# Optimization experiments

Measured on AMD Instinct MI355X. Metric: run time of the kernel, lower is better.

## Reference

```python
import jax, jax.numpy as jnp
import numpy as np

L = 2048      # seq_len
E = 2048      # hidden_dim
H = 16        # num_heads
D = E // H    # head_dim


def setup_inputs() -> dict:
    key = jax.random.key(0)
    ks = jax.random.split(key, 6)
    x = jax.random.normal(ks[0], (L, E), dtype=jnp.float32)
    bias_matrix = jax.random.normal(ks[1], (L, L), dtype=jnp.float32) * 0.1
    # nn.MultiheadAttention params: packed in_proj [3E, E] + bias [3E], out_proj [E, E] + bias [E]
    in_proj_weight = jax.random.normal(ks[2], (3 * E, E), dtype=jnp.float32) * 0.02
    in_proj_bias = jax.random.normal(ks[3], (3 * E,), dtype=jnp.float32) * 0.02
    out_proj_weight = jax.random.normal(ks[4], (E, E), dtype=jnp.float32) * 0.02
    out_proj_bias = jax.random.normal(ks[5], (E,), dtype=jnp.float32) * 0.02
    return {
        "x": x,
        "bias_matrix": bias_matrix,
        "in_proj_weight": in_proj_weight,
        "in_proj_bias": in_proj_bias,
        "out_proj_weight": out_proj_weight,
        "out_proj_bias": out_proj_bias,
    }


def reference(x, bias_matrix, in_proj_weight, in_proj_bias, out_proj_weight, out_proj_bias):
    # Packed QKV projection (torch Linear convention: y = x @ W.T + b)
    qkv = x @ in_proj_weight.T + in_proj_bias            # [L, 3E]
    q, k, v = jnp.split(qkv, 3, axis=-1)                 # each [L, E]
    q = q.reshape(L, H, D)
    k = k.reshape(L, H, D)
    v = v.reshape(L, H, D)
    scale = 1.0 / jnp.sqrt(jnp.asarray(D, dtype=x.dtype))
    # scores: [H, L, L]; bias_matrix broadcast over heads (torch 2D attn_mask semantics)
    scores = jnp.einsum("lhd,mhd->hlm", q * scale, k) + bias_matrix[None, :, :]
    attn = jax.nn.softmax(scores, axis=-1)
    ctx = jnp.einsum("hlm,mhd->lhd", attn, v).reshape(L, E)
    out = ctx @ out_proj_weight.T + out_proj_bias        # [L, E]
    return out
```

## Files before the change

### kernel.cpp

```cpp
#include <hip/hip_runtime.h>
#include <math.h>

#define L_SEQ 2048
#define E_DIM 2048
#define H_NUM 16
#define D_HEAD 128

typedef __attribute__((ext_vector_type(8))) _Float16 half8;
typedef __attribute__((ext_vector_type(4))) _Float16 half4;
typedef __attribute__((ext_vector_type(4))) float floatx4;

static __device__ __forceinline__ void gload16(const void* g, void* lds) {
  __builtin_amdgcn_global_load_lds(
      (const __attribute__((address_space(1))) void*)g,
      (__attribute__((address_space(3))) void*)lds, 16, 0, 0);
}

__global__ __launch_bounds__(256)
void cvt3_f32_f16(const float* __restrict__ a, _Float16* __restrict__ oa, int na,
                  const float* __restrict__ b, _Float16* __restrict__ ob, int nb,
                  const float* __restrict__ c, _Float16* __restrict__ oc, int nc) {
  int i = (blockIdx.x * 256 + threadIdx.x) * 8;
  const float* src;
  _Float16* dst;
  if (i < na) {
    src = a + i; dst = oa + i;
  } else if (i < na + nb) {
    src = b + (i - na); dst = ob + (i - na);
  } else if (i < na + nb + nc) {
    src = c + (i - na - nb); dst = oc + (i - na - nb);
  } else {
    return;
  }
  float4 p = *(const float4*)src;
  float4 q = *(const float4*)(src + 4);
  half8 h = {(_Float16)p.x, (_Float16)p.y, (_Float16)p.z, (_Float16)p.w,
             (_Float16)q.x, (_Float16)q.y, (_Float16)q.z, (_Float16)q.w};
  *(half8*)dst = h;
}

template <int TM, int TN, int WR, int WC, int EPI>
__global__ __launch_bounds__(256)
void gemm_mfma(const _Float16* __restrict__ A, const _Float16* __restrict__ B,
               const float* __restrict__ bias, float* __restrict__ C,
               _Float16* __restrict__ qk, _Float16* __restrict__ vt,
               int M, int N, int K) {
  constexpr int RT = TM / (16 * WR);
  constexpr int CT = TN / (16 * WC);
  constexpr int ACH = TM / 8;
  constexpr int NCH = (TM + TN) / 32;

  __shared__ _Float16 As[TM * 64];
  __shared__ _Float16 Bs[TN * 64];

  const int tid = threadIdx.x;
  const int wave = tid >> 6, lane = tid & 63;
  const int l15 = lane & 15, quad = lane >> 4;
  const int wr = wave / WC, wc = wave % WC;
  const int row0 = blockIdx.y * TM, col0 = blockIdx.x * TN;

  const int srow = lane >> 3;
  const int gc = (lane & 7) ^ srow;

  floatx4 acc[RT][CT];
#pragma unroll
  for (int i = 0; i < RT; ++i)
#pragma unroll
    for (int j = 0; j < CT; ++j) acc[i][j] = (floatx4){0.f, 0.f, 0.f, 0.f};

  for (int k0 = 0; k0 < K; k0 += 64) {
    __syncthreads();
#pragma unroll
    for (int c = 0; c < NCH; ++c) {
      int chunk = wave * NCH + c;
      if (chunk < ACH) {
        int row = chunk * 8 + srow;
        gload16((const char*)(A + (size_t)(row0 + row) * K + k0) + gc * 16,
                (char*)As + chunk * 1024);
      } else {
        int bch = chunk - ACH;
        int row = bch * 8 + srow;
        gload16((const char*)(B + (size_t)(col0 + row) * K + k0) + gc * 16,
                (char*)Bs + bch * 1024);
      }
    }
    __syncthreads();

#pragma unroll
    for (int ks = 0; ks < 2; ++ks) {
      half8 af[RT], bf[CT];
#pragma unroll
      for (int t = 0; t < RT; ++t) {
        int r = wr * (16 * RT) + t * 16 + l15;
        af[t] = *(const half8*)&As[r * 64 + (((ks * 4 + quad) ^ (r & 7)) * 8)];
      }
#pragma unroll
      for (int t = 0; t < CT; ++t) {
        int r = wc * (16 * CT) + t * 16 + l15;
        bf[t] = *(const half8*)&Bs[r * 64 + (((ks * 4 + quad) ^ (r & 7)) * 8)];
      }
#pragma unroll
      for (int tr = 0; tr < RT; ++tr)
#pragma unroll
        for (int tc = 0; tc < CT; ++tc)
          acc[tr][tc] = __builtin_amdgcn_mfma_f32_16x16x32_f16(
              af[tr], bf[tc], acc[tr][tc], 0, 0, 0);
    }
  }

  const int crow = row0 + wr * (16 * RT);
  const int ccol = col0 + wc * (16 * CT);

  if (EPI == 0) {
#pragma unroll
    for (int tc = 0; tc < CT; ++tc) {
      int col = ccol + tc * 16 + l15;
      float bb = bias[col];
#pragma unroll
      for (int tr = 0; tr < RT; ++tr)
#pragma unroll
        for (int r = 0; r < 4; ++r)
          C[(size_t)(crow + tr * 16 + quad * 4 + r) * N + col] =
              acc[tr][tc][r] + bb;
    }
  } else if (col0 < 2 * E_DIM) {
#pragma unroll
    for (int tc = 0; tc < CT; ++tc) {
      int col = ccol + tc * 16 + l15;
      float bb = bias[col];
#pragma unroll
      for (int tr = 0; tr < RT; ++tr)
#pragma unroll
        for (int r = 0; r < 4; ++r)
          qk[(size_t)(crow + tr * 16 + quad * 4 + r) * (2 * E_DIM) + col] =
              (_Float16)(acc[tr][tc][r] + bb);
    }
  } else {
#pragma unroll
    for (int tc = 0; tc < CT; ++tc) {
      int col = ccol + tc * 16 + l15;
      float bb = bias[col];
      int vrow = col - 2 * E_DIM;
#pragma unroll
      for (int tr = 0; tr < RT; ++tr) {
        int rbase = crow + tr * 16 + quad * 4;
        half4 h = {(_Float16)(acc[tr][tc][0] + bb), (_Float16)(acc[tr][tc][1] + bb),
                   (_Float16)(acc[tr][tc][2] + bb), (_Float16)(acc[tr][tc][3] + bb)};
        *(half4*)&vt[(size_t)vrow * L_SEQ + rbase] = h;
      }
    }
  }
}

__global__ __launch_bounds__(256, 1)
void attn_mfma(const _Float16* __restrict__ qk, const _Float16* __restrict__ vt,
               const float* __restrict__ bias, _Float16* __restrict__ ctx) {
  const int h = blockIdx.y;
  const int q0 = blockIdx.x * 128;
  const int tid = threadIdx.x;
  const int wave = tid >> 6;
  const int lane = tid & 63;
  const int l15 = lane & 15;
  const int quad = lane >> 4;

  __shared__ _Float16 Ks[64][136];
  __shared__ _Float16 Vst[128][72];
  __shared__ _Float16 Ps[128][72];

  half8 qa[2][4];
#pragma unroll
  for (int rt = 0; rt < 2; ++rt) {
    const _Float16* qp = qk + (size_t)(q0 + wave * 32 + rt * 16 + l15) * (2 * E_DIM) +
                         h * D_HEAD + quad * 8;
#pragma unroll
    for (int ks = 0; ks < 4; ++ks) qa[rt][ks] = *(const half8*)(qp + ks * 32);
  }

  float l_i[2][4];
#pragma unroll
  for (int rt = 0; rt < 2; ++rt)
#pragma unroll
    for (int r = 0; r < 4; ++r) l_i[rt][r] = 0.f;
  floatx4 o[2][8];
#pragma unroll
  for (int rt = 0; rt < 2; ++rt)
#pragma unroll
    for (int t = 0; t < 8; ++t) o[rt][t] = (floatx4){0.f, 0.f, 0.f, 0.f};

  const float scale = 0.088388347648318447f;

  half8 kreg[4], vreg[4];
  float breg[2][4][4], breg2[2][4][4];
#pragma unroll
  for (int c = 0; c < 4; ++c) {
    int m = c * 256 + tid;
    kreg[c] = *(const half8*)(qk + (size_t)(0 + (m >> 4)) * (2 * E_DIM) + E_DIM +
                              h * D_HEAD + (m & 15) * 8);
    vreg[c] = *(const half8*)(vt + (size_t)(h * D_HEAD + (m >> 3)) * L_SEQ + 0 +
                              (m & 7) * 8);
  }
#pragma unroll
  for (int rt = 0; rt < 2; ++rt)
#pragma unroll
    for (int t = 0; t < 4; ++t)
#pragma unroll
      for (int r = 0; r < 4; ++r)
        breg[rt][t][r] = bias[(size_t)(q0 + wave * 32 + rt * 16 + quad * 4 + r) *
                                  L_SEQ + 16 * t + l15];

#pragma unroll 2
  for (int kt = 0; kt < L_SEQ; kt += 64) {
    __syncthreads();
#pragma unroll
    for (int c = 0; c < 4; ++c) {
      int m = c * 256 + tid;
      *(half8*)&Ks[m >> 4][(m & 15) * 8] = kreg[c];
      *(half8*)&Vst[m >> 3][(m & 7) * 8] = vreg[c];
    }
    __syncthreads();

    if (kt + 64 < L_SEQ) {
#pragma unroll
      for (int c = 0; c < 4; ++c) {
        int m = c * 256 + tid;
        kreg[c] = *(const half8*)(qk + (size_t)(kt + 64 + (m >> 4)) * (2 * E_DIM) +
                                  E_DIM + h * D_HEAD + (m & 15) * 8);
        vreg[c] = *(const half8*)(vt + (size_t)(h * D_HEAD + (m >> 3)) * L_SEQ +
                                  kt + 64 + (m & 7) * 8);
      }
#pragma unroll
      for (int rt = 0; rt < 2; ++rt)
#pragma unroll
        for (int t = 0; t < 4; ++t)
#pragma unroll
          for (int r = 0; r < 4; ++r)
            breg2[rt][t][r] =
                bias[(size_t)(q0 + wave * 32 + rt * 16 + quad * 4 + r) * L_SEQ +
                     kt + 64 + 16 * t + l15];
    }

    floatx4 s[2][4];
#pragma unroll
    for (int t = 0; t < 4; ++t) {
      floatx4 a0 = (floatx4){0.f, 0.f, 0.f, 0.f};
      floatx4 a1 = (floatx4){0.f, 0.f, 0.f, 0.f};
#pragma unroll
      for (int ks = 0; ks < 4; ++ks) {
        half8 b = *(const half8*)&Ks[16 * t + l15][ks * 32 + quad * 8];
        a0 = __builtin_amdgcn_mfma_f32_16x16x32_f16(qa[0][ks], b, a0, 0, 0, 0);
        a1 = __builtin_amdgcn_mfma_f32_16x16x32_f16(qa[1][ks], b, a1, 0, 0, 0);
      }
      s[0][t] = a0;
      s[1][t] = a1;
    }

#pragma unroll
    for (int rt = 0; rt < 2; ++rt)
#pragma unroll
      for (int t = 0; t < 4; ++t)
#pragma unroll
        for (int r = 0; r < 4; ++r) {
          float p = __expf(fmaf(s[rt][t][r], scale, breg[rt][t][r]));
          s[rt][t][r] = p;
          Ps[wave * 32 + rt * 16 + quad * 4 + r][16 * t + l15] = (_Float16)p;
        }
#pragma unroll
    for (int rt = 0; rt < 2; ++rt)
#pragma unroll
      for (int r = 0; r < 4; ++r) {
        float ls = s[rt][0][r] + s[rt][1][r] + s[rt][2][r] + s[rt][3][r];
        ls += __shfl_xor(ls, 1);
        ls += __shfl_xor(ls, 2);
        ls += __shfl_xor(ls, 4);
        ls += __shfl_xor(ls, 8);
        l_i[rt][r] += ls;
      }

    half8 pa[2][2];
#pragma unroll
    for (int rt = 0; rt < 2; ++rt)
#pragma unroll
      for (int ks = 0; ks < 2; ++ks)
        pa[rt][ks] = *(const half8*)&Ps[wave * 32 + rt * 16 + l15][ks * 32 + quad * 8];
#pragma unroll
    for (int t = 0; t < 8; ++t) {
#pragma unroll
      for (int ks = 0; ks < 2; ++ks) {
        half8 b = *(const half8*)&Vst[16 * t + l15][ks * 32 + quad * 8];
        o[0][t] = __builtin_amdgcn_mfma_f32_16x16x32_f16(pa[0][ks], b, o[0][t], 0, 0, 0);
        o[1][t] = __builtin_amdgcn_mfma_f32_16x16x32_f16(pa[1][ks], b, o[1][t], 0, 0, 0);
      }
    }

#pragma unroll
    for (int rt = 0; rt < 2; ++rt)
#pragma unroll
      for (int t = 0; t < 4; ++t)
#pragma unroll
        for (int r = 0; r < 4; ++r) breg[rt][t][r] = breg2[rt][t][r];
  }

#pragma unroll
  for (int rt = 0; rt < 2; ++rt) {
    float inv_l[4];
#pragma unroll
    for (int r = 0; r < 4; ++r) inv_l[r] = 1.f / l_i[rt][r];
#pragma unroll
    for (int t = 0; t < 8; ++t)
#pragma unroll
      for (int r = 0; r < 4; ++r) {
        int row = q0 + wave * 32 + rt * 16 + quad * 4 + r;
        ctx[(size_t)row * E_DIM + h * D_HEAD + 16 * t + l15] =
            (_Float16)(o[rt][t][r] * inv_l[r]);
      }
  }
}

extern "C" void kernel_launch(void* const* d_in, const int* in_sizes, int n_in,
                              void* d_out, int out_size, void* d_ws, size_t ws_size,
                              hipStream_t stream) {
  const float* x          = (const float*)d_in[0];
  const float* bias_mat   = (const float*)d_in[1];
  const float* in_proj_w  = (const float*)d_in[2];
  const float* in_proj_b  = (const float*)d_in[3];
  const float* out_proj_w = (const float*)d_in[4];
  const float* out_proj_b = (const float*)d_in[5];
  float* out = (float*)d_out;

  _Float16* x16 = (_Float16*)d_ws;
  _Float16* w1  = x16 + (size_t)L_SEQ * E_DIM;
  _Float16* w2  = w1 + (size_t)3 * E_DIM * E_DIM;
  _Float16* qk  = w2 + (size_t)E_DIM * E_DIM;
  _Float16* vt  = qk + (size_t)L_SEQ * 2 * E_DIM;
  _Float16* ctx = vt + (size_t)E_DIM * L_SEQ;

  dim3 blk(256);
  const int nx = L_SEQ * E_DIM, nw1 = 3 * E_DIM * E_DIM, nw2 = E_DIM * E_DIM;

  cvt3_f32_f16<<<(nx + nw1 + nw2) / 2048, blk, 0, stream>>>(
      x, x16, nx, in_proj_w, w1, nw1, out_proj_w, w2, nw2);

  gemm_mfma<128, 128, 2, 2, 1><<<dim3(3 * E_DIM / 128, L_SEQ / 128), blk, 0, stream>>>(
      x16, w1, in_proj_b, nullptr, qk, vt, L_SEQ, 3 * E_DIM, E_DIM);

  attn_mfma<<<dim3(L_SEQ / 128, H_NUM), blk, 0, stream>>>(qk, vt, bias_mat, ctx);

  gemm_mfma<128, 64, 4, 1, 0><<<dim3(E_DIM / 64, L_SEQ / 128), blk, 0, stream>>>(
      ctx, w2, out_proj_b, out, nullptr, nullptr, L_SEQ, E_DIM, E_DIM);
}
```

Measured before the change: 342.5 us.

## Split attention over two key halves and merge partial results in a combine kernel

```diff
diff --git a/kernel.cpp b/kernel.cpp
--- a/kernel.cpp
+++ b/kernel.cpp
@@ -152,11 +152,15 @@
   }
 }
 
-__global__ __launch_bounds__(256, 1)
+__global__ __launch_bounds__(256, 2)
 void attn_mfma(const _Float16* __restrict__ qk, const _Float16* __restrict__ vt,
-               const float* __restrict__ bias, _Float16* __restrict__ ctx) {
+               const float* __restrict__ bias, _Float16* __restrict__ o_part,
+               float* __restrict__ l_part) {
   const int h = blockIdx.y;
   const int q0 = blockIdx.x * 128;
+  const int z = blockIdx.z;
+  const int kbase = z * (L_SEQ / 2);
+  const int kend = kbase + (L_SEQ / 2);
   const int tid = threadIdx.x;
   const int wave = tid >> 6;
   const int lane = tid & 63;
@@ -194,9 +198,9 @@
 #pragma unroll
   for (int c = 0; c < 4; ++c) {
     int m = c * 256 + tid;
-    kreg[c] = *(const half8*)(qk + (size_t)(0 + (m >> 4)) * (2 * E_DIM) + E_DIM +
+    kreg[c] = *(const half8*)(qk + (size_t)(kbase + (m >> 4)) * (2 * E_DIM) + E_DIM +
                               h * D_HEAD + (m & 15) * 8);
-    vreg[c] = *(const half8*)(vt + (size_t)(h * D_HEAD + (m >> 3)) * L_SEQ + 0 +
+    vreg[c] = *(const half8*)(vt + (size_t)(h * D_HEAD + (m >> 3)) * L_SEQ + kbase +
                               (m & 7) * 8);
   }
 #pragma unroll
@@ -206,10 +210,10 @@
 #pragma unroll
       for (int r = 0; r < 4; ++r)
         breg[rt][t][r] = bias[(size_t)(q0 + wave * 32 + rt * 16 + quad * 4 + r) *
-                                  L_SEQ + 16 * t + l15];
+                                  L_SEQ + kbase + 16 * t + l15];
 
 #pragma unroll 2
-  for (int kt = 0; kt < L_SEQ; kt += 64) {
+  for (int kt = kbase; kt < kend; kt += 64) {
     __syncthreads();
 #pragma unroll
     for (int c = 0; c < 4; ++c) {
@@ -219,7 +223,7 @@
     }
     __syncthreads();
 
-    if (kt + 64 < L_SEQ) {
+    if (kt + 64 < kend) {
 #pragma unroll
       for (int c = 0; c < 4; ++c) {
         int m = c * 256 + tid;
@@ -302,18 +306,40 @@
 
 #pragma unroll
   for (int rt = 0; rt < 2; ++rt) {
-    float inv_l[4];
-#pragma unroll
-    for (int r = 0; r < 4; ++r) inv_l[r] = 1.f / l_i[rt][r];
 #pragma unroll
     for (int t = 0; t < 8; ++t)
 #pragma unroll
       for (int r = 0; r < 4; ++r) {
         int row = q0 + wave * 32 + rt * 16 + quad * 4 + r;
-        ctx[(size_t)row * E_DIM + h * D_HEAD + 16 * t + l15] =
-            (_Float16)(o[rt][t][r] * inv_l[r]);
-      }
-  }
+        o_part[((size_t)z * L_SEQ + row) * E_DIM + h * D_HEAD + 16 * t + l15] =
+            (_Float16)o[rt][t][r];
+      }
+    if (l15 == 0) {
+#pragma unroll
+      for (int r = 0; r < 4; ++r) {
+        int row = q0 + wave * 32 + rt * 16 + quad * 4 + r;
+        l_part[((size_t)z * H_NUM + h) * L_SEQ + row] = l_i[rt][r];
+      }
+    }
+  }
+}
+
+__global__ __launch_bounds__(256)
+void attn_combine(const _Float16* __restrict__ o_part,
+                  const float* __restrict__ l_part, _Float16* __restrict__ ctx) {
+  size_t i = ((size_t)blockIdx.x * 256 + threadIdx.x) * 8;
+  int q = (int)(i / E_DIM);
+  int col = (int)(i % E_DIM);
+  int h = col >> 7;
+  float l = l_part[h * L_SEQ + q] + l_part[(size_t)H_NUM * L_SEQ + h * L_SEQ + q];
+  float inv = 1.f / l;
+  half8 a = *(const half8*)(o_part + i);
+  half8 b = *(const half8*)(o_part + (size_t)L_SEQ * E_DIM + i);
+  half8 o;
+#pragma unroll
+  for (int k = 0; k < 8; ++k)
+    o[k] = (_Float16)(((float)a[k] + (float)b[k]) * inv);
+  *(half8*)(ctx + i) = o;
 }
 
 extern "C" void kernel_launch(void* const* d_in, const int* in_sizes, int n_in,
@@ -333,6 +359,8 @@
   _Float16* qk  = w2 + (size_t)E_DIM * E_DIM;
   _Float16* vt  = qk + (size_t)L_SEQ * 2 * E_DIM;
   _Float16* ctx = vt + (size_t)E_DIM * L_SEQ;
+  float* l_part = (float*)(ctx + (size_t)L_SEQ * E_DIM);
+  _Float16* o_part = x16;
 
   dim3 blk(256);
   const int nx = L_SEQ * E_DIM, nw1 = 3 * E_DIM * E_DIM, nw2 = E_DIM * E_DIM;
@@ -343,7 +371,10 @@
   gemm_mfma<128, 128, 2, 2, 1><<<dim3(3 * E_DIM / 128, L_SEQ / 128), blk, 0, stream>>>(
       x16, w1, in_proj_b, nullptr, qk, vt, L_SEQ, 3 * E_DIM, E_DIM);
 
-  attn_mfma<<<dim3(L_SEQ / 128, H_NUM), blk, 0, stream>>>(qk, vt, bias_mat, ctx);
+  attn_mfma<<<dim3(L_SEQ / 128, H_NUM, 2), blk, 0, stream>>>(qk, vt, bias_mat,
+                                                             o_part, l_part);
+
+  attn_combine<<<(L_SEQ * E_DIM) / 2048, blk, 0, stream>>>(o_part, l_part, ctx);
 
   gemm_mfma<128, 64, 4, 1, 0><<<dim3(E_DIM / 64, L_SEQ / 128), blk, 0, stream>>>(
       ctx, w2, out_proj_b, out, nullptr, nullptr, L_SEQ, E_DIM, E_DIM);
```

Result: slower. 397.2 us (+16.0%).

## Double-buffer K/V tiles, transpose score MFMA, and read bias as fp16

Applied to the files above, without the earlier changes.

```diff
diff --git a/kernel.cpp b/kernel.cpp
--- a/kernel.cpp
+++ b/kernel.cpp
@@ -39,6 +39,17 @@
   *(half8*)dst = h;
 }
 
+__global__ __launch_bounds__(256)
+void cvt_f32_f16(const float* __restrict__ in, _Float16* __restrict__ out, int n) {
+  int i = (blockIdx.x * 256 + threadIdx.x) * 8;
+  if (i >= n) return;
+  float4 a = *(const float4*)(in + i);
+  float4 b = *(const float4*)(in + i + 4);
+  half8 h = {(_Float16)a.x, (_Float16)a.y, (_Float16)a.z, (_Float16)a.w,
+             (_Float16)b.x, (_Float16)b.y, (_Float16)b.z, (_Float16)b.w};
+  *(half8*)(out + i) = h;
+}
+
 template <int TM, int TN, int WR, int WC, int EPI>
 __global__ __launch_bounds__(256)
 void gemm_mfma(const _Float16* __restrict__ A, const _Float16* __restrict__ B,
@@ -154,17 +165,17 @@
 
 __global__ __launch_bounds__(256, 1)
 void attn_mfma(const _Float16* __restrict__ qk, const _Float16* __restrict__ vt,
-               const float* __restrict__ bias, _Float16* __restrict__ ctx) {
-  const int h = blockIdx.y;
-  const int q0 = blockIdx.x * 128;
+               const _Float16* __restrict__ bias16, _Float16* __restrict__ ctx) {
+  const int h = blockIdx.x;
+  const int q0 = blockIdx.y * 128;
   const int tid = threadIdx.x;
   const int wave = tid >> 6;
   const int lane = tid & 63;
   const int l15 = lane & 15;
   const int quad = lane >> 4;
 
-  __shared__ _Float16 Ks[64][136];
-  __shared__ _Float16 Vst[128][72];
+  __shared__ _Float16 Ks[2][64][136];
+  __shared__ _Float16 Vst[2][128][72];
   __shared__ _Float16 Ps[128][72];
 
   half8 qa[2][4];
@@ -176,50 +187,45 @@
     for (int ks = 0; ks < 4; ++ks) qa[rt][ks] = *(const half8*)(qp + ks * 32);
   }
 
-  float l_i[2][4];
+  float l_i[2] = {0.f, 0.f};
+  floatx4 o[2][8];
 #pragma unroll
   for (int rt = 0; rt < 2; ++rt)
 #pragma unroll
-    for (int r = 0; r < 4; ++r) l_i[rt][r] = 0.f;
-  floatx4 o[2][8];
-#pragma unroll
-  for (int rt = 0; rt < 2; ++rt)
-#pragma unroll
     for (int t = 0; t < 8; ++t) o[rt][t] = (floatx4){0.f, 0.f, 0.f, 0.f};
 
   const float scale = 0.088388347648318447f;
 
   half8 kreg[4], vreg[4];
-  float breg[2][4][4], breg2[2][4][4];
+  half4 bcur[2][4], bnxt[2][4];
 #pragma unroll
   for (int c = 0; c < 4; ++c) {
     int m = c * 256 + tid;
-    kreg[c] = *(const half8*)(qk + (size_t)(0 + (m >> 4)) * (2 * E_DIM) + E_DIM +
+    kreg[c] = *(const half8*)(qk + (size_t)(m >> 4) * (2 * E_DIM) + E_DIM +
                               h * D_HEAD + (m & 15) * 8);
-    vreg[c] = *(const half8*)(vt + (size_t)(h * D_HEAD + (m >> 3)) * L_SEQ + 0 +
+    vreg[c] = *(const half8*)(vt + (size_t)(h * D_HEAD + (m >> 3)) * L_SEQ +
                               (m & 7) * 8);
   }
 #pragma unroll
   for (int rt = 0; rt < 2; ++rt)
 #pragma unroll
     for (int t = 0; t < 4; ++t)
-#pragma unroll
-      for (int r = 0; r < 4; ++r)
-        breg[rt][t][r] = bias[(size_t)(q0 + wave * 32 + rt * 16 + quad * 4 + r) *
-                                  L_SEQ + 16 * t + l15];
+      bcur[rt][t] = *(const half4*)&bias16[(size_t)(q0 + wave * 32 + rt * 16 + l15) *
+                                               L_SEQ + 16 * t + quad * 4];
+#pragma unroll
+  for (int c = 0; c < 4; ++c) {
+    int m = c * 256 + tid;
+    *(half8*)&Ks[0][m >> 4][(m & 15) * 8] = kreg[c];
+    *(half8*)&Vst[0][m >> 3][(m & 7) * 8] = vreg[c];
+  }
 
 #pragma unroll 2
-  for (int kt = 0; kt < L_SEQ; kt += 64) {
+  for (int it = 0; it < 32; ++it) {
+    const int cur = it & 1, nxt = cur ^ 1;
+    const int kt = it * 64;
     __syncthreads();
-#pragma unroll
-    for (int c = 0; c < 4; ++c) {
-      int m = c * 256 + tid;
-      *(half8*)&Ks[m >> 4][(m & 15) * 8] = kreg[c];
-      *(half8*)&Vst[m >> 3][(m & 7) * 8] = vreg[c];
-    }
-    __syncthreads();
-
-    if (kt + 64 < L_SEQ) {
+
+    if (it < 31) {
 #pragma unroll
       for (int c = 0; c < 4; ++c) {
         int m = c * 256 + tid;
@@ -232,49 +238,48 @@
       for (int rt = 0; rt < 2; ++rt)
 #pragma unroll
         for (int t = 0; t < 4; ++t)
-#pragma unroll
-          for (int r = 0; r < 4; ++r)
-            breg2[rt][t][r] =
-                bias[(size_t)(q0 + wave * 32 + rt * 16 + quad * 4 + r) * L_SEQ +
-                     kt + 64 + 16 * t + l15];
-    }
-
-    floatx4 s[2][4];
+          bnxt[rt][t] =
+              *(const half4*)&bias16[(size_t)(q0 + wave * 32 + rt * 16 + l15) *
+                                         L_SEQ + kt + 64 + 16 * t + quad * 4];
+    }
+
+    floatx4 st[2][4];
 #pragma unroll
     for (int t = 0; t < 4; ++t) {
-      floatx4 a0 = (floatx4){0.f, 0.f, 0.f, 0.f};
-      floatx4 a1 = (floatx4){0.f, 0.f, 0.f, 0.f};
-#pragma unroll
-      for (int ks = 0; ks < 4; ++ks) {
-        half8 b = *(const half8*)&Ks[16 * t + l15][ks * 32 + quad * 8];
-        a0 = __builtin_amdgcn_mfma_f32_16x16x32_f16(qa[0][ks], b, a0, 0, 0, 0);
-        a1 = __builtin_amdgcn_mfma_f32_16x16x32_f16(qa[1][ks], b, a1, 0, 0, 0);
-      }
-      s[0][t] = a0;
-      s[1][t] = a1;
-    }
-
-#pragma unroll
-    for (int rt = 0; rt < 2; ++rt)
+      st[0][t] = (floatx4){0.f, 0.f, 0.f, 0.f};
+      st[1][t] = (floatx4){0.f, 0.f, 0.f, 0.f};
+    }
+#pragma unroll
+    for (int ks = 0; ks < 4; ++ks)
+#pragma unroll
+      for (int t = 0; t < 4; ++t) {
+        half8 kf = *(const half8*)&Ks[cur][16 * t + l15][ks * 32 + quad * 8];
+        st[0][t] = __builtin_amdgcn_mfma_f32_16x16x32_f16(kf, qa[0][ks], st[0][t], 0, 0, 0);
+        st[1][t] = __builtin_amdgcn_mfma_f32_16x16x32_f16(kf, qa[1][ks], st[1][t], 0, 0, 0);
+      }
+
+#pragma unroll
+    for (int rt = 0; rt < 2; ++rt) {
+      float ls = 0.f;
+      float ps[4][4];
 #pragma unroll
       for (int t = 0; t < 4; ++t)
 #pragma unroll
         for (int r = 0; r < 4; ++r) {
-          float p = __expf(fmaf(s[rt][t][r], scale, breg[rt][t][r]));
-          s[rt][t][r] = p;
-          Ps[wave * 32 + rt * 16 + quad * 4 + r][16 * t + l15] = (_Float16)p;
+          float p = __expf(fmaf(st[rt][t][r], scale, (float)bcur[rt][t][r]));
+          ps[t][r] = p;
+          ls += p;
         }
-#pragma unroll
-    for (int rt = 0; rt < 2; ++rt)
-#pragma unroll
-      for (int r = 0; r < 4; ++r) {
-        float ls = s[rt][0][r] + s[rt][1][r] + s[rt][2][r] + s[rt][3][r];
-        ls += __shfl_xor(ls, 1);
-        ls += __shfl_xor(ls, 2);
-        ls += __shfl_xor(ls, 4);
-        ls += __shfl_xor(ls, 8);
-        l_i[rt][r] += ls;
-      }
+      ls += __shfl_xor(ls, 16);
+      ls += __shfl_xor(ls, 32);
+      l_i[rt] += ls;
+#pragma unroll
+      for (int t = 0; t < 4; ++t) {
+        half4 hp = {(_Float16)ps[t][0], (_Float16)ps[t][1],
+                    (_Float16)ps[t][2], (_Float16)ps[t][3]};
+        *(half4*)&Ps[wave * 32 + rt * 16 + l15][16 * t + quad * 4] = hp;
+      }
+    }
 
     half8 pa[2][2];
 #pragma unroll
@@ -286,32 +291,38 @@
     for (int t = 0; t < 8; ++t) {
 #pragma unroll
       for (int ks = 0; ks < 2; ++ks) {
-        half8 b = *(const half8*)&Vst[16 * t + l15][ks * 32 + quad * 8];
-        o[0][t] = __builtin_amdgcn_mfma_f32_16x16x32_f16(pa[0][ks], b, o[0][t], 0, 0, 0);
-        o[1][t] = __builtin_amdgcn_mfma_f32_16x16x32_f16(pa[1][ks], b, o[1][t], 0, 0, 0);
-      }
-    }
-
-#pragma unroll
-    for (int rt = 0; rt < 2; ++rt)
-#pragma unroll
-      for (int t = 0; t < 4; ++t)
-#pragma unroll
-        for (int r = 0; r < 4; ++r) breg[rt][t][r] = breg2[rt][t][r];
+        half8 vf = *(const half8*)&Vst[cur][16 * t + l15][ks * 32 + quad * 8];
+        o[0][t] = __builtin_amdgcn_mfma_f32_16x16x32_f16(pa[0][ks], vf, o[0][t], 0, 0, 0);
+        o[1][t] = __builtin_amdgcn_mfma_f32_16x16x32_f16(pa[1][ks], vf, o[1][t], 0, 0, 0);
+      }
+    }
+
+    if (it < 31) {
+#pragma unroll
+      for (int c = 0; c < 4; ++c) {
+        int m = c * 256 + tid;
+        *(half8*)&Ks[nxt][m >> 4][(m & 15) * 8] = kreg[c];
+        *(half8*)&Vst[nxt][m >> 3][(m & 7) * 8] = vreg[c];
+      }
+#pragma unroll
+      for (int rt = 0; rt < 2; ++rt)
+#pragma unroll
+        for (int t = 0; t < 4; ++t) bcur[rt][t] = bnxt[rt][t];
+    }
   }
 
 #pragma unroll
   for (int rt = 0; rt < 2; ++rt) {
-    float inv_l[4];
-#pragma unroll
-    for (int r = 0; r < 4; ++r) inv_l[r] = 1.f / l_i[rt][r];
+    float inv[4];
+#pragma unroll
+    for (int r = 0; r < 4; ++r) inv[r] = 1.f / __shfl(l_i[rt], quad * 4 + r);
 #pragma unroll
     for (int t = 0; t < 8; ++t)
 #pragma unroll
       for (int r = 0; r < 4; ++r) {
         int row = q0 + wave * 32 + rt * 16 + quad * 4 + r;
         ctx[(size_t)row * E_DIM + h * D_HEAD + 16 * t + l15] =
-            (_Float16)(o[rt][t][r] * inv_l[r]);
+            (_Float16)(o[rt][t][r] * inv[r]);
       }
   }
 }
@@ -333,6 +344,7 @@
   _Float16* qk  = w2 + (size_t)E_DIM * E_DIM;
   _Float16* vt  = qk + (size_t)L_SEQ * 2 * E_DIM;
   _Float16* ctx = vt + (size_t)E_DIM * L_SEQ;
+  _Float16* bias16 = x16;
 
   dim3 blk(256);
   const int nx = L_SEQ * E_DIM, nw1 = 3 * E_DIM * E_DIM, nw2 = E_DIM * E_DIM;
@@ -343,7 +355,10 @@
   gemm_mfma<128, 128, 2, 2, 1><<<dim3(3 * E_DIM / 128, L_SEQ / 128), blk, 0, stream>>>(
       x16, w1, in_proj_b, nullptr, qk, vt, L_SEQ, 3 * E_DIM, E_DIM);
 
-  attn_mfma<<<dim3(L_SEQ / 128, H_NUM), blk, 0, stream>>>(qk, vt, bias_mat, ctx);
+  cvt_f32_f16<<<(L_SEQ * L_SEQ) / 2048, blk, 0, stream>>>(bias_mat, bias16,
+                                                          L_SEQ * L_SEQ);
+
+  attn_mfma<<<dim3(H_NUM, L_SEQ / 128), blk, 0, stream>>>(qk, vt, bias16, ctx);
 
   gemm_mfma<128, 64, 4, 1, 0><<<dim3(E_DIM / 64, L_SEQ / 128), blk, 0, stream>>>(
       ctx, w2, out_proj_b, out, nullptr, nullptr, L_SEQ, E_DIM, E_DIM);
```

After: 312.3 us. -8.8%, faster.
